# Performance work log

Hardware: AMD Instinct MI355X
Metric: run time of the kernel (lower is better)

The kernel has to match this reference:

```python
import jax, jax.numpy as jnp
import numpy as np

N, D, H, E = 4096, 512, 8, 131072
DH = D // H
BN_EPS = 1e-5


def setup_inputs() -> dict:
    key = jax.random.key(0)
    ks = jax.random.split(key, 12)
    def w(k, shape):
        return jax.random.normal(k, shape, dtype=jnp.float32) * 0.02
    return {
        'x': jax.random.normal(ks[0], (N, D), dtype=jnp.float32),
        'edge_index': jax.random.randint(ks[1], (2, E), 0, N),
        'edge_attr': jax.random.normal(ks[2], (E, D), dtype=jnp.float32),
        # GINE MLP: Linear(D,D) -> ReLU -> Linear(D,D)  (torch layout [out,in])
        'w_gin1': w(ks[3], (D, D)), 'b_gin1': jnp.zeros((D,), jnp.float32),
        'w_gin2': w(ks[4], (D, D)), 'b_gin2': jnp.zeros((D,), jnp.float32),
        # MultiheadAttention in/out projections
        'w_qkv': w(ks[5], (3 * D, D)), 'b_qkv': jnp.zeros((3 * D,), jnp.float32),
        'w_o': w(ks[6], (D, D)), 'b_o': jnp.zeros((D,), jnp.float32),
        # BatchNorm affine params
        'bn1l_g': jnp.ones((D,), jnp.float32), 'bn1l_b': jnp.zeros((D,), jnp.float32),
        'bn1a_g': jnp.ones((D,), jnp.float32), 'bn1a_b': jnp.zeros((D,), jnp.float32),
        # FFN: D -> 2D -> D
        'w_ff1': w(ks[7], (2 * D, D)), 'b_ff1': jnp.zeros((2 * D,), jnp.float32),
        'w_ff2': w(ks[8], (D, 2 * D)), 'b_ff2': jnp.zeros((D,), jnp.float32),
        'bn2_g': jnp.ones((D,), jnp.float32), 'bn2_b': jnp.zeros((D,), jnp.float32),
    }


def _bn(x, g, b):
    # BatchNorm1d in training mode: batch statistics over the node dim
    m = jnp.mean(x, axis=0)
    v = jnp.var(x, axis=0)
    return (x - m) * jax.lax.rsqrt(v + BN_EPS) * g + b


def _forward(x, edge_index, edge_attr,
             w_gin1, b_gin1, w_gin2, b_gin2,
             w_qkv, b_qkv, w_o, b_o,
             bn1l_g, bn1l_b, bn1a_g, bn1a_b,
             w_ff1, b_ff1, w_ff2, b_ff2, bn2_g, bn2_b):
    h_in = x
    src, dst = edge_index[0], edge_index[1]
    # --- local GINEConv: nn((1+eps)*x + sum_j relu(x_j + e_ji)), eps=0 ---
    msg = jax.nn.relu(x[src] + edge_attr)                       # [E, D]
    agg = jax.ops.segment_sum(msg, dst, num_segments=N)         # [N, D]
    gin_h = x + agg
    h_local = jax.nn.relu(gin_h @ w_gin1.T + b_gin1) @ w_gin2.T + b_gin2
    h_local = _bn(h_in + h_local, bn1l_g, bn1l_b)               # residual + BN
    # --- global multi-head self-attention over all nodes (single graph) ---
    qkv = x @ w_qkv.T + b_qkv                                   # [N, 3D]
    q, k, v = jnp.split(qkv, 3, axis=-1)
    q = q.reshape(N, H, DH).transpose(1, 0, 2)                  # [H, N, DH]
    k = k.reshape(N, H, DH).transpose(1, 0, 2)
    v = v.reshape(N, H, DH).transpose(1, 0, 2)
    scores = jnp.einsum('hnd,hmd->hnm', q, k) / np.float32(np.sqrt(DH))
    attn = jax.nn.softmax(scores, axis=-1)                      # [H, N, N]
    o = jnp.einsum('hnm,hmd->hnd', attn, v).transpose(1, 0, 2).reshape(N, D)
    h_attn = _bn(h_in + (o @ w_o.T + b_o), bn1a_g, bn1a_b)
    # --- combine branches + FFN block ---
    h = h_local + h_attn
    h = h + (jax.nn.relu(h @ w_ff1.T + b_ff1) @ w_ff2.T + b_ff2)
    return _bn(h, bn2_g, bn2_b)


def reference(x, edge_index, edge_attr,
              w_gin1, b_gin1, w_gin2, b_gin2,
              w_qkv, b_qkv, w_o, b_o,
              bn1l_g, bn1l_b, bn1a_g, bn1a_b,
              w_ff1, b_ff1, w_ff2, b_ff2, bn2_g, bn2_b):
    return _forward(x, edge_index, edge_attr,
                    w_gin1, b_gin1, w_gin2, b_gin2,
                    w_qkv, b_qkv, w_o, b_o,
                    bn1l_g, bn1l_b, bn1a_g, bn1a_b,
                    w_ff1, b_ff1, w_ff2, b_ff2, bn2_g, bn2_b)
```

## Files before the change

kernel.cpp:

```cpp
#include <hip/hip_runtime.h>

#define Nn 4096
#define Dd 512
#define Hh 8
#define Ee 131072
#define DEGCAP 96

typedef __attribute__((ext_vector_type(8))) short short8v;
typedef __attribute__((ext_vector_type(8))) unsigned short ushort8v;
typedef __attribute__((ext_vector_type(4))) short short4v;
typedef __attribute__((ext_vector_type(4))) float f32x4v;
typedef __attribute__((ext_vector_type(4))) unsigned short ushort4v;

__device__ __forceinline__ float bf2f(unsigned short u) {
    return __uint_as_float(((unsigned int)u) << 16);
}
__device__ __forceinline__ unsigned short f2bf(float f) {
    unsigned int u = __float_as_uint(f);
    return (unsigned short)((u + 0x7fff + ((u >> 16) & 1)) >> 16);
}
__device__ __forceinline__ void gl_lds16(const void* g, void* l) {
    __builtin_amdgcn_global_load_lds((const __attribute__((address_space(1))) void*)g,
                                     (__attribute__((address_space(3))) void*)l, 16, 0, 0);
}

struct CastJobs {
    const float* src[6];
    unsigned short* dst[6];
    int start[7];
    int* cnt;
    float* stats;
};

__global__ __launch_bounds__(256) void cast_multi(CastJobs cj) {
    int gid = blockIdx.x * 256 + threadIdx.x;
    if (gid < 4096) cj.cnt[gid] = 0;
    if (gid < 6144) cj.stats[gid] = 0.f;
    int b = blockIdx.x;
    int j = 0;
    while (b >= cj.start[j + 1]) j++;
    int off = (b - cj.start[j]) * 1024 + threadIdx.x * 4;
    f32x4v v = *(const f32x4v*)(cj.src[j] + off);
    ushort4v o;
    o.x = f2bf(v.x); o.y = f2bf(v.y); o.z = f2bf(v.z); o.w = f2bf(v.w);
    *(ushort4v*)(cj.dst[j] + off) = o;
}

__global__ __launch_bounds__(256) void edge_scatter(const int* __restrict__ ei,
                                                    int* __restrict__ cnt,
                                                    int* __restrict__ eidx) {
    int e = blockIdx.x * 256 + threadIdx.x;
    int d = ei[Ee + e];
    int pos = atomicAdd(&cnt[d], 1);
    if (pos < DEGCAP) eidx[d * DEGCAP + pos] = e;
}

__global__ __launch_bounds__(256) void gine_gather(const float* __restrict__ x,
                                                   const int* __restrict__ ei,
                                                   const float* __restrict__ ea,
                                                   const int* __restrict__ cnt,
                                                   const int* __restrict__ eidx,
                                                   unsigned short* __restrict__ gh,
                                                   unsigned short* __restrict__ xb) {
    __shared__ int se[DEGCAP];
    __shared__ int ss[DEGCAP];
    __shared__ float part[512];
    const int node = blockIdx.x;
    const int t = threadIdx.x;
    const int deg = min(cnt[node], DEGCAP);
    const int tc = t & 127, ep = t >> 7;

    if (t < deg) {
        int e = eidx[node * DEGCAP + t];
        se[t] = e;
        ss[t] = ei[e];
    }
    __syncthreads();

    f32x4v acc = {0.f, 0.f, 0.f, 0.f};
    int k = ep;
    while (k + 2 < deg) {
        int e0 = se[k], s0 = ss[k];
        int e1 = se[k + 2], s1 = ss[k + 2];
        f32x4v ev0 = *(const f32x4v*)(ea + (size_t)e0 * Dd + tc * 4);
        f32x4v xv0 = *(const f32x4v*)(x + (size_t)s0 * Dd + tc * 4);
        f32x4v ev1 = *(const f32x4v*)(ea + (size_t)e1 * Dd + tc * 4);
        f32x4v xv1 = *(const f32x4v*)(x + (size_t)s1 * Dd + tc * 4);
#pragma unroll
        for (int i = 0; i < 4; i++) {
            acc[i] += fmaxf(xv0[i] + ev0[i], 0.f);
            acc[i] += fmaxf(xv1[i] + ev1[i], 0.f);
        }
        k += 4;
    }
    if (k < deg) {
        int e0 = se[k], s0 = ss[k];
        f32x4v ev0 = *(const f32x4v*)(ea + (size_t)e0 * Dd + tc * 4);
        f32x4v xv0 = *(const f32x4v*)(x + (size_t)s0 * Dd + tc * 4);
#pragma unroll
        for (int i = 0; i < 4; i++) acc[i] += fmaxf(xv0[i] + ev0[i], 0.f);
    }

    if (ep) *(f32x4v*)&part[tc * 4] = acc;
    __syncthreads();
    if (!ep) {
        f32x4v o = *(const f32x4v*)&part[tc * 4];
        f32x4v xd = *(const f32x4v*)(x + (size_t)node * Dd + tc * 4);
        ushort4v ov, xv;
#pragma unroll
        for (int i = 0; i < 4; i++) {
            ov[i] = f2bf(xd[i] + acc[i] + o[i]);
            xv[i] = f2bf(xd[i]);
        }
        *(ushort4v*)(gh + (size_t)node * Dd + tc * 4) = ov;
        *(ushort4v*)(xb + (size_t)node * Dd + tc * 4) = xv;
    }
}

template <int K, int MB, bool RELU, bool OUTBF16, int RESMODE, bool SXADD, int SOFF, bool ACOMB>
__device__ __forceinline__ void gemm_body(char* smem,
                                          const short* __restrict__ A,
                                          const short* __restrict__ B,
                                          const float* __restrict__ bias,
                                          const void* __restrict__ res,
                                          void* __restrict__ outp, int Nc,
                                          const float* __restrict__ sx,
                                          float* __restrict__ stats,
                                          const unsigned short* __restrict__ op0,
                                          const unsigned short* __restrict__ op1,
                                          const unsigned short* __restrict__ op2,
                                          const unsigned short* __restrict__ op3,
                                          const float* __restrict__ lsum,
                                          int bx, int by, int t) {
    constexpr int BM = MB * 32;
    short* lA = (short*)smem;
    short* lB = (short*)(smem + MB * 2048);
    float* sst = (float*)(smem + MB * 2048 + 8192);
    const int lane = t & 63, w = t >> 6;
    const int wr = w >> 1, wc = w & 1;
    const int l15 = lane & 15, lhi = lane >> 4;
    const int m0 = by * BM, n0 = bx * 128;
    f32x4v acc[MB][4] = {};
    const int c0 = t, c1 = t + 256;

    for (int k0 = 0; k0 < K; k0 += 32) {
        __syncthreads();
        if constexpr (ACOMB) {
            int r = c0 >> 2, s = c0 & 3;
            int row = m0 + r;
            int kb = k0 + s * 8;
            int h = k0 >> 6;
            float inv = 1.f / (lsum[(size_t)h * Nn + row] + lsum[(size_t)(Hh + h) * Nn + row] +
                               lsum[(size_t)(2 * Hh + h) * Nn + row] + lsum[(size_t)(3 * Hh + h) * Nn + row]);
            ushort8v p0 = *(const ushort8v*)&op0[(size_t)row * 512 + kb];
            ushort8v p1 = *(const ushort8v*)&op1[(size_t)row * 512 + kb];
            ushort8v p2 = *(const ushort8v*)&op2[(size_t)row * 512 + kb];
            ushort8v p3 = *(const ushort8v*)&op3[(size_t)row * 512 + kb];
            short8v ov;
#pragma unroll
            for (int i = 0; i < 8; i++)
                ov[i] = (short)f2bf((bf2f(p0[i]) + bf2f(p1[i]) + bf2f(p2[i]) + bf2f(p3[i])) * inv);
            *(short8v*)((char*)lA + c0 * 16) = ov;
        } else {
            gl_lds16(A + (size_t)(m0 + (c0 >> 2)) * K + k0 + (c0 & 3) * 8, (char*)lA + c0 * 16);
            if constexpr (MB == 4)
                gl_lds16(A + (size_t)(m0 + (c1 >> 2)) * K + k0 + (c1 & 3) * 8, (char*)lA + c1 * 16);
        }
        gl_lds16(B + (size_t)(n0 + (c0 >> 2)) * K + k0 + (c0 & 3) * 8, (char*)lB + c0 * 16);
        gl_lds16(B + (size_t)(n0 + (c1 >> 2)) * K + k0 + (c1 & 3) * 8, (char*)lB + c1 * 16);
        __syncthreads();
        short8v af[MB], bf[4];
#pragma unroll
        for (int m = 0; m < MB; m++)
            af[m] = *(const short8v*)&lA[(wr * (MB * 16) + m * 16 + l15) * 32 + lhi * 8];
#pragma unroll
        for (int n = 0; n < 4; n++)
            bf[n] = *(const short8v*)&lB[(wc * 64 + n * 16 + l15) * 32 + lhi * 8];
#pragma unroll
        for (int m = 0; m < MB; m++)
#pragma unroll
            for (int n = 0; n < 4; n++)
                acc[m][n] = __builtin_amdgcn_mfma_f32_16x16x32_bf16(af[m], bf[n], acc[m][n], 0, 0, 0);
    }

    float csum[4] = {0.f, 0.f, 0.f, 0.f}, cssq[4] = {0.f, 0.f, 0.f, 0.f};

#pragma unroll
    for (int m = 0; m < MB; m++)
#pragma unroll
        for (int n = 0; n < 4; n++)
#pragma unroll
            for (int j = 0; j < 4; j++) {
                int col = n0 + wc * 64 + n * 16 + l15;
                int row = m0 + wr * (MB * 16) + m * 16 + lhi * 4 + j;
                size_t idx = (size_t)row * Nc + col;
                float v = acc[m][n][j] + bias[col];
                if (RELU) v = fmaxf(v, 0.f);
                if constexpr (RESMODE == 1) v += ((const float*)res)[idx];
                if constexpr (RESMODE == 2) v += bf2f(((const unsigned short*)res)[idx]);
                if constexpr (SOFF >= 0) {
                    float a = SXADD ? (sx[idx] + v) : v;
                    csum[n] += a;
                    cssq[n] += a * a;
                }
                if (OUTBF16)
                    ((unsigned short*)outp)[idx] = f2bf(v);
                else
                    ((float*)outp)[idx] = v;
            }

    if constexpr (SOFF >= 0) {
        sst[t] = 0.f;
        __syncthreads();
#pragma unroll
        for (int n = 0; n < 4; n++) {
            float s = csum[n], q = cssq[n];
            s += __shfl_xor(s, 16); s += __shfl_xor(s, 32);
            q += __shfl_xor(q, 16); q += __shfl_xor(q, 32);
            if (lhi == 0) {
                int c = wc * 64 + n * 16 + l15;
                atomicAdd(&sst[c * 2], s);
                atomicAdd(&sst[c * 2 + 1], q);
            }
        }
        __syncthreads();
        atomicAdd(&stats[SOFF + (t & 1) * 512 + n0 + (t >> 1)], sst[t]);
    }
}

__device__ __forceinline__ void attn_body(char* smem, const short* __restrict__ qkv,
                                          unsigned short* __restrict__ op0,
                                          unsigned short* __restrict__ op1,
                                          unsigned short* __restrict__ op2,
                                          unsigned short* __restrict__ op3,
                                          float* __restrict__ lsum,
                                          int bx, int by, int t) {
    const int lane = t & 63, w = t >> 6;
    const int h = by >> 2, quarter = by & 3;
    const int kvbase = quarter * 1024;
    const int qw = bx * 256 + w * 64;
    const int l15 = lane & 15, lhi = lane >> 4;
    const int ksw = l15 & 7;
    const int qs3 = (l15 >> 1) & 7;
    unsigned short* __restrict__ opart = quarter == 0 ? op0 : quarter == 1 ? op1 : quarter == 2 ? op2 : op3;

    short* pP = (short*)(smem + 32768) + w * 4096;

    short8v qf[4][2];
#pragma unroll
    for (int g = 0; g < 4; g++)
#pragma unroll
        for (int kk = 0; kk < 2; kk++)
            qf[g][kk] = *(const short8v*)&qkv[(size_t)(qw + g * 16 + l15) * 1536 + h * 64 + kk * 32 + lhi * 8];

    f32x4v oacc[4][4] = {};
    float lrow[4] = {0.f, 0.f, 0.f, 0.f};
    const float SC2 = 0.125f * 1.44269504f;

    int kidx[4][2];
#pragma unroll
    for (int r = 0; r < 4; r++)
#pragma unroll
        for (int kk = 0; kk < 2; kk++)
            kidx[r][kk] = (l15 + r * 16) * 64 + (((kk * 4 + lhi) ^ ksw) * 8);

    int pw_idx[4], prd_idx[2];
#pragma unroll
    for (int c2 = 0; c2 < 4; c2++)
        pw_idx[c2] = l15 * 64 + (((c2 * 2 + (lhi >> 1)) ^ qs3) * 8) + ((lhi & 1) * 4);
#pragma unroll
    for (int c = 0; c < 2; c++)
        prd_idx[c] = l15 * 64 + (((c * 4 + lhi) ^ qs3) * 8);

    unsigned vbase0 = (unsigned)(size_t)(smem + 16384) + lhi * 256 + l15 * 2;

    auto stage = [&](int kt, int b) {
        int kv0 = kvbase + kt * 64;
#pragma unroll
        for (int i = 0; i < 2; i++) {
            gl_lds16(qkv + (size_t)(kv0 + (t >> 3) + 32 * i) * 1536 + 512 + h * 64 + ((t & 7) ^ ((t >> 3) & 7)) * 8,
                     smem + b * 8192 + t * 16 + i * 4096);
        }
#pragma unroll
        for (int i = 0; i < 2; i++) {
            int db = (t >> 7) + 2 * i;
            int kv = (t >> 1) & 63;
            int dh_in = (t & 1) * 8;
            gl_lds16(qkv + (size_t)(kv0 + kv) * 1536 + 1024 + h * 64 + db * 16 + dh_in,
                     smem + 16384 + b * 8192 + t * 16 + i * 4096);
        }
    };

    stage(0, 0);
    __syncthreads();

    for (int kt = 0; kt < 16; kt++) {
        const int b = kt & 1;
        if (kt + 1 < 16) stage(kt + 1, b ^ 1);

        const short* Kb = (const short*)smem + b * 4096;
        const unsigned vbase = vbase0 + b * 8192;

        f32x4v s[4][4] = {};
        __builtin_amdgcn_s_setprio(1);
#pragma unroll
        for (int r = 0; r < 4; r++) {
            short8v k0 = *(const short8v*)&Kb[kidx[r][0]];
            short8v k1 = *(const short8v*)&Kb[kidx[r][1]];
#pragma unroll
            for (int g = 0; g < 4; g++) {
                s[g][r] = __builtin_amdgcn_mfma_f32_16x16x32_bf16(k0, qf[g][0], s[g][r], 0, 0, 0);
                s[g][r] = __builtin_amdgcn_mfma_f32_16x16x32_bf16(k1, qf[g][1], s[g][r], 0, 0, 0);
            }
        }
        __builtin_amdgcn_s_setprio(0);

#pragma unroll
        for (int g = 0; g < 4; g++) {
            float p[16];
            float rs = 0.f;
#pragma unroll
            for (int r = 0; r < 4; r++)
#pragma unroll
                for (int j = 0; j < 4; j++) {
                    float e = exp2f(fmaf(s[g][r][j], SC2, -4.f));
                    p[r * 4 + j] = e;
                    rs += e;
                }
            rs += __shfl_xor(rs, 16);
            rs += __shfl_xor(rs, 32);
            lrow[g] += rs;

            short* pPg = pP + g * 1024;
#pragma unroll
            for (int c2 = 0; c2 < 4; c2++) {
                short4v pk;
#pragma unroll
                for (int j = 0; j < 4; j++) pk[j] = (short)f2bf(p[c2 * 4 + j]);
                *(short4v*)&pPg[pw_idx[c2]] = pk;
            }
        }
        asm volatile("" ::: "memory");

        short8v pf[4][2];
#pragma unroll
        for (int g = 0; g < 4; g++)
#pragma unroll
            for (int c = 0; c < 2; c++)
                pf[g][c] = *(const short8v*)&pP[g * 1024 + prd_idx[c]];

        short4v v00a, v00b, v01a, v01b, v10a, v10b, v11a, v11b;
        short4v v20a, v20b, v21a, v21b, v30a, v30b, v31a, v31b;
        asm volatile("ds_read_b64_tr_b16 %0, %1" : "=v"(v00a) : "v"(vbase));
        asm volatile("ds_read_b64_tr_b16 %0, %1 offset:128" : "=v"(v00b) : "v"(vbase));
        asm volatile("ds_read_b64_tr_b16 %0, %1 offset:1024" : "=v"(v01a) : "v"(vbase));
        asm volatile("ds_read_b64_tr_b16 %0, %1 offset:1152" : "=v"(v01b) : "v"(vbase));
        asm volatile("ds_read_b64_tr_b16 %0, %1 offset:2048" : "=v"(v10a) : "v"(vbase));
        asm volatile("ds_read_b64_tr_b16 %0, %1 offset:2176" : "=v"(v10b) : "v"(vbase));
        asm volatile("ds_read_b64_tr_b16 %0, %1 offset:3072" : "=v"(v11a) : "v"(vbase));
        asm volatile("ds_read_b64_tr_b16 %0, %1 offset:3200" : "=v"(v11b) : "v"(vbase));
        asm volatile("ds_read_b64_tr_b16 %0, %1 offset:4096" : "=v"(v20a) : "v"(vbase));
        asm volatile("ds_read_b64_tr_b16 %0, %1 offset:4224" : "=v"(v20b) : "v"(vbase));
        asm volatile("ds_read_b64_tr_b16 %0, %1 offset:5120" : "=v"(v21a) : "v"(vbase));
        asm volatile("ds_read_b64_tr_b16 %0, %1 offset:5248" : "=v"(v21b) : "v"(vbase));
        asm volatile("ds_read_b64_tr_b16 %0, %1 offset:6144" : "=v"(v30a) : "v"(vbase));
        asm volatile("ds_read_b64_tr_b16 %0, %1 offset:6272" : "=v"(v30b) : "v"(vbase));
        asm volatile("ds_read_b64_tr_b16 %0, %1 offset:7168" : "=v"(v31a) : "v"(vbase));
        asm volatile("ds_read_b64_tr_b16 %0, %1 offset:7296" : "=v"(v31b) : "v"(vbase));

        asm volatile("s_waitcnt lgkmcnt(0)" ::: "memory");
        __builtin_amdgcn_sched_barrier(0);

#define VFCAT(a, b) __builtin_shufflevector(a, b, 0, 1, 2, 3, 4, 5, 6, 7)
        short8v vv[4][2];
        vv[0][0] = VFCAT(v00a, v00b); vv[0][1] = VFCAT(v01a, v01b);
        vv[1][0] = VFCAT(v10a, v10b); vv[1][1] = VFCAT(v11a, v11b);
        vv[2][0] = VFCAT(v20a, v20b); vv[2][1] = VFCAT(v21a, v21b);
        vv[3][0] = VFCAT(v30a, v30b); vv[3][1] = VFCAT(v31a, v31b);
#undef VFCAT
        __builtin_amdgcn_s_setprio(1);
#pragma unroll
        for (int g = 0; g < 4; g++)
#pragma unroll
            for (int n = 0; n < 4; n++) {
                oacc[g][n] = __builtin_amdgcn_mfma_f32_16x16x32_bf16(pf[g][0], vv[n][0], oacc[g][n], 0, 0, 0);
                oacc[g][n] = __builtin_amdgcn_mfma_f32_16x16x32_bf16(pf[g][1], vv[n][1], oacc[g][n], 0, 0, 0);
            }
        __builtin_amdgcn_s_setprio(0);

        __syncthreads();
    }

#pragma unroll
    for (int g = 0; g < 4; g++) {
#pragma unroll
        for (int j = 0; j < 4; j++) {
            int row = qw + g * 16 + lhi * 4 + j;
#pragma unroll
            for (int n = 0; n < 4; n++)
                opart[(size_t)row * Dd + h * 64 + n * 16 + l15] = f2bf(oacc[g][n][j]);
        }
        if (lhi == 0)
            lsum[(size_t)(quarter * Hh + h) * Nn + qw + g * 16 + l15] = lrow[g];
    }
}

__global__ __launch_bounds__(256) void gin1_qkv(const short* ginh, const short* wg1b,
                                                const float* b_gin1, unsigned short* t1,
                                                const short* xb, const short* wqkvb,
                                                const float* b_qkv, unsigned short* qkvb) {
    __shared__ char smem[16384];
    int b = blockIdx.x, t = threadIdx.x;
    if (b < 256) {
        gemm_body<512, 2, true, true, 0, false, -1, false>(
            smem, ginh, wg1b, b_gin1, nullptr, t1, 512, nullptr, nullptr,
            nullptr, nullptr, nullptr, nullptr, nullptr, b & 3, b >> 2, t);
    } else {
        int bb = b - 256;
        gemm_body<512, 4, false, true, 0, false, -1, false>(
            smem, xb, wqkvb, b_qkv, nullptr, qkvb, 1536, nullptr, nullptr,
            nullptr, nullptr, nullptr, nullptr, nullptr, bb % 12, bb / 12, t);
    }
}

__global__ __launch_bounds__(256, 2) void gin2_attn(const short* qkvb, unsigned short* op0,
                                                    unsigned short* op1, unsigned short* op2,
                                                    unsigned short* op3, float* lsum,
                                                    const short* t1, const short* wg2b,
                                                    const float* b_gin2, float* hlp,
                                                    const float* x, float* stats) {
    __shared__ char smem[65536];
    int b = blockIdx.x, t = threadIdx.x;
    if (b < 512) {
        attn_body(smem, qkvb, op0, op1, op2, op3, lsum, b & 15, b >> 4, t);
    } else {
        int bb = b - 512;
        gemm_body<512, 2, false, false, 0, true, 0, false>(
            smem, t1, wg2b, b_gin2, nullptr, hlp, 512, x, stats,
            nullptr, nullptr, nullptr, nullptr, nullptr, bb & 3, bb >> 2, t);
    }
}

__global__ __launch_bounds__(256) void oproj_fused(const short* wob, const float* b_o,
                                                   float* attn_pre, const float* x, float* stats,
                                                   const unsigned short* op0,
                                                   const unsigned short* op1,
                                                   const unsigned short* op2,
                                                   const unsigned short* op3,
                                                   const float* lsum) {
    __shared__ char smem[13312];
    gemm_body<512, 2, false, false, 0, true, 1024, true>(
        smem, nullptr, wob, b_o, nullptr, attn_pre, 512, x, stats,
        op0, op1, op2, op3, lsum, blockIdx.x, blockIdx.y, threadIdx.x);
}

__global__ __launch_bounds__(256) void ff1_k(const short* hb, const short* wf1b,
                                             const float* b_ff1, unsigned short* t2) {
    __shared__ char smem[16384];
    gemm_body<512, 4, true, true, 0, false, -1, false>(
        smem, hb, wf1b, b_ff1, nullptr, t2, 1024, nullptr, nullptr,
        nullptr, nullptr, nullptr, nullptr, nullptr, blockIdx.x, blockIdx.y, threadIdx.x);
}

__global__ __launch_bounds__(256) void ff2_k(const short* t2, const short* wf2b,
                                             const float* b_ff2, const unsigned short* hb,
                                             float* dout, float* stats) {
    __shared__ char smem[13312];
    gemm_body<1024, 2, false, false, 2, false, 4096, false>(
        smem, t2, wf2b, b_ff2, hb, dout, 512, nullptr, stats,
        nullptr, nullptr, nullptr, nullptr, nullptr, blockIdx.x, blockIdx.y, threadIdx.x);
}

__global__ __launch_bounds__(256) void bn_combine(const float* __restrict__ x,
                                                  const float* __restrict__ p1,
                                                  const float* __restrict__ p2,
                                                  const float* __restrict__ stats,
                                                  const float* __restrict__ g1,
                                                  const float* __restrict__ b1,
                                                  const float* __restrict__ g2,
                                                  const float* __restrict__ b2,
                                                  unsigned short* __restrict__ hb) {
    int i0 = (blockIdx.x * 256 + threadIdx.x) * 4;
    int c0 = i0 & 511;
    f32x4v xv = *(const f32x4v*)(x + i0);
    f32x4v av = *(const f32x4v*)(p1 + i0);
    f32x4v bv = *(const f32x4v*)(p2 + i0);
    ushort4v hbv;
#pragma unroll
    for (int e = 0; e < 4; e++) {
        int c = c0 + e;
        float ma = stats[c] * (1.f / Nn);
        float va = stats[512 + c] * (1.f / Nn) - ma * ma;
        float sA = g1[c] * rsqrtf(va + 1e-5f);
        float bA = b1[c] - ma * sA;
        float mb = stats[1024 + c] * (1.f / Nn);
        float vb = stats[1536 + c] * (1.f / Nn) - mb * mb;
        float sB = g2[c] * rsqrtf(vb + 1e-5f);
        float bB = b2[c] - mb * sB;
        float a = xv[e] + av[e];
        float b = xv[e] + bv[e];
        hbv[e] = f2bf(a * sA + bA + b * sB + bB);
    }
    *(ushort4v*)(hb + i0) = hbv;
}

__global__ __launch_bounds__(256) void bn_apply(float* __restrict__ out,
                                                const float* __restrict__ stats,
                                                const float* __restrict__ g,
                                                const float* __restrict__ b) {
    int i0 = (blockIdx.x * 256 + threadIdx.x) * 4;
    int c0 = i0 & 511;
    f32x4v v = *(const f32x4v*)(out + i0);
#pragma unroll
    for (int e = 0; e < 4; e++) {
        int c = c0 + e;
        float m = stats[4096 + c] * (1.f / Nn);
        float va = stats[4608 + c] * (1.f / Nn) - m * m;
        float s = g[c] * rsqrtf(va + 1e-5f);
        v[e] = (v[e] - m) * s + b[c];
    }
    *(f32x4v*)(out + i0) = v;
}

extern "C" void kernel_launch(void* const* d_in, const int* in_sizes, int n_in,
                              void* d_out, int out_size, void* d_ws, size_t ws_size,
                              hipStream_t stream) {
    const float* x = (const float*)d_in[0];
    const int* ei = (const int*)d_in[1];
    const float* ea = (const float*)d_in[2];
    const float* w_gin1 = (const float*)d_in[3];
    const float* b_gin1 = (const float*)d_in[4];
    const float* w_gin2 = (const float*)d_in[5];
    const float* b_gin2 = (const float*)d_in[6];
    const float* w_qkv = (const float*)d_in[7];
    const float* b_qkv = (const float*)d_in[8];
    const float* w_o = (const float*)d_in[9];
    const float* b_o = (const float*)d_in[10];
    const float* bn1l_g = (const float*)d_in[11];
    const float* bn1l_b = (const float*)d_in[12];
    const float* bn1a_g = (const float*)d_in[13];
    const float* bn1a_b = (const float*)d_in[14];
    const float* w_ff1 = (const float*)d_in[15];
    const float* b_ff1 = (const float*)d_in[16];
    const float* w_ff2 = (const float*)d_in[17];
    const float* b_ff2 = (const float*)d_in[18];
    const float* bn2_g = (const float*)d_in[19];
    const float* bn2_b = (const float*)d_in[20];

    char* ws = (char*)d_ws;
    unsigned short* wg1b = (unsigned short*)(ws + 0);
    unsigned short* wg2b = (unsigned short*)(ws + 524288);
    unsigned short* wqkvb = (unsigned short*)(ws + 1048576);
    unsigned short* wob = (unsigned short*)(ws + 2621440);
    unsigned short* wf1b = (unsigned short*)(ws + 3145728);
    unsigned short* wf2b = (unsigned short*)(ws + 4194304);
    unsigned short* xb = (unsigned short*)(ws + 5242880);
    unsigned short* qkvb = (unsigned short*)(ws + 9437184);
    int* eidx = (int*)(ws + 22020096);
    int* cnt = (int*)(ws + 23592960);
    unsigned short* ginh = (unsigned short*)(ws + 30408704);
    float* lsum = (float*)(ws + 30408704);
    unsigned short* t1 = (unsigned short*)(ws + 34603008);
    float* hlp = (float*)(ws + 38797312);
    unsigned short* opart2 = (unsigned short*)(ws + 47185920);
    float* attn_pre = (float*)(ws + 51380224);
    unsigned short* opart0 = (unsigned short*)(ws + 59768832);
    unsigned short* hb = (unsigned short*)(ws + 68157440);
    unsigned short* opart3 = (unsigned short*)(ws + 68157440);
    unsigned short* t2 = (unsigned short*)(ws + 72351744);
    unsigned short* opart1 = (unsigned short*)(ws + 72351744);
    float* stats = (float*)(ws + 80740352);

    CastJobs cj;
    cj.src[0] = w_gin1; cj.dst[0] = wg1b;
    cj.src[1] = w_gin2; cj.dst[1] = wg2b;
    cj.src[2] = w_qkv;  cj.dst[2] = wqkvb;
    cj.src[3] = w_o;    cj.dst[3] = wob;
    cj.src[4] = w_ff1;  cj.dst[4] = wf1b;
    cj.src[5] = w_ff2;  cj.dst[5] = wf2b;
    cj.cnt = cnt;
    cj.stats = stats;
    int nelem[6] = {Dd * Dd, Dd * Dd, 3 * Dd * Dd, Dd * Dd, 2 * Dd * Dd, 2 * Dd * Dd};
    cj.start[0] = 0;
    for (int i = 0; i < 6; i++) cj.start[i + 1] = cj.start[i] + nelem[i] / 1024;
    cast_multi<<<cj.start[6], 256, 0, stream>>>(cj);

    edge_scatter<<<Ee / 256, 256, 0, stream>>>(ei, cnt, eidx);
    gine_gather<<<Nn, 256, 0, stream>>>(x, ei, ea, cnt, eidx, ginh, xb);

    gin1_qkv<<<640, 256, 0, stream>>>((const short*)ginh, (const short*)wg1b, b_gin1, t1,
                                      (const short*)xb, (const short*)wqkvb, b_qkv, qkvb);

    gin2_attn<<<768, 256, 0, stream>>>((const short*)qkvb, opart0, opart1, opart2, opart3, lsum,
                                       (const short*)t1, (const short*)wg2b, b_gin2, hlp,
                                       x, stats);

    oproj_fused<<<dim3(4, 64), 256, 0, stream>>>((const short*)wob, b_o, attn_pre, x, stats,
                                                 opart0, opart1, opart2, opart3, lsum);

    bn_combine<<<Nn * Dd / 1024, 256, 0, stream>>>(x, hlp, attn_pre, stats,
                                                   bn1l_g, bn1l_b, bn1a_g, bn1a_b, hb);

    ff1_k<<<dim3(8, 32), 256, 0, stream>>>((const short*)hb, (const short*)wf1b, b_ff1, t2);
    ff2_k<<<dim3(4, 64), 256, 0, stream>>>((const short*)t2, (const short*)wf2b, b_ff2,
                                           hb, (float*)d_out, stats);

    bn_apply<<<Nn * Dd / 1024, 256, 0, stream>>>((float*)d_out, stats, bn2_g, bn2_b);
}
```

Before: 257.2 us.

## Load attention K fragments directly from global into registers, shrink LDS

Each wave now loads its K-tile MFMA operands straight from global memory into double-buffered registers, prefetching the next tile, instead of staging K through LDS. Only V is still staged in LDS, so shared memory drops from 64KB to 48KB and the P buffer moves down. Launch bounds lose the minimum-2-blocks hint. This removes the LDS writes and reads for K, but each wave now issues redundant global/L2 reads of K and uses more registers, which may lower occupancy.

```diff
diff --git a/kernel.cpp b/kernel.cpp
--- a/kernel.cpp
+++ b/kernel.cpp
@@ -240,11 +240,10 @@
     const int kvbase = quarter * 1024;
     const int qw = bx * 256 + w * 64;
     const int l15 = lane & 15, lhi = lane >> 4;
-    const int ksw = l15 & 7;
     const int qs3 = (l15 >> 1) & 7;
     unsigned short* __restrict__ opart = quarter == 0 ? op0 : quarter == 1 ? op1 : quarter == 2 ? op2 : op3;
 
-    short* pP = (short*)(smem + 32768) + w * 4096;
+    short* pP = (short*)(smem + 16384) + w * 4096;
 
     short8v qf[4][2];
 #pragma unroll
@@ -257,12 +256,12 @@
     float lrow[4] = {0.f, 0.f, 0.f, 0.f};
     const float SC2 = 0.125f * 1.44269504f;
 
-    int kidx[4][2];
+    const short* kp[4][2];
 #pragma unroll
     for (int r = 0; r < 4; r++)
 #pragma unroll
         for (int kk = 0; kk < 2; kk++)
-            kidx[r][kk] = (l15 + r * 16) * 64 + (((kk * 4 + lhi) ^ ksw) * 8);
+            kp[r][kk] = qkv + (size_t)(kvbase + l15 + r * 16) * 1536 + 512 + h * 64 + kk * 32 + lhi * 8;
 
     int pw_idx[4], prd_idx[2];
 #pragma unroll
@@ -272,47 +271,49 @@
     for (int c = 0; c < 2; c++)
         prd_idx[c] = l15 * 64 + (((c * 4 + lhi) ^ qs3) * 8);
 
-    unsigned vbase0 = (unsigned)(size_t)(smem + 16384) + lhi * 256 + l15 * 2;
-
-    auto stage = [&](int kt, int b) {
+    unsigned vbase0 = (unsigned)(size_t)smem + lhi * 256 + l15 * 2;
+
+    auto stageV = [&](int kt, int b) {
         int kv0 = kvbase + kt * 64;
-#pragma unroll
-        for (int i = 0; i < 2; i++) {
-            gl_lds16(qkv + (size_t)(kv0 + (t >> 3) + 32 * i) * 1536 + 512 + h * 64 + ((t & 7) ^ ((t >> 3) & 7)) * 8,
-                     smem + b * 8192 + t * 16 + i * 4096);
-        }
 #pragma unroll
         for (int i = 0; i < 2; i++) {
             int db = (t >> 7) + 2 * i;
             int kv = (t >> 1) & 63;
             int dh_in = (t & 1) * 8;
             gl_lds16(qkv + (size_t)(kv0 + kv) * 1536 + 1024 + h * 64 + db * 16 + dh_in,
-                     smem + 16384 + b * 8192 + t * 16 + i * 4096);
+                     smem + b * 8192 + t * 16 + i * 4096);
         }
     };
-
-    stage(0, 0);
+    auto loadK = [&](int kt, short8v (&kf)[4][2]) {
+        size_t roff = (size_t)kt * 64 * 1536;
+#pragma unroll
+        for (int r = 0; r < 4; r++)
+#pragma unroll
+            for (int kk = 0; kk < 2; kk++)
+                kf[r][kk] = *(const short8v*)(kp[r][kk] + roff);
+    };
+
+    short8v kfA[4][2], kfB[4][2];
+    loadK(0, kfA);
+    stageV(0, 0);
     __syncthreads();
 
-    for (int kt = 0; kt < 16; kt++) {
-        const int b = kt & 1;
-        if (kt + 1 < 16) stage(kt + 1, b ^ 1);
-
-        const short* Kb = (const short*)smem + b * 4096;
+    auto body = [&](int kt, int b, short8v (&kfC)[4][2], short8v (&kfN)[4][2]) {
+        if (kt + 1 < 16) {
+            loadK(kt + 1, kfN);
+            stageV(kt + 1, b ^ 1);
+        }
         const unsigned vbase = vbase0 + b * 8192;
 
         f32x4v s[4][4] = {};
         __builtin_amdgcn_s_setprio(1);
 #pragma unroll
-        for (int r = 0; r < 4; r++) {
-            short8v k0 = *(const short8v*)&Kb[kidx[r][0]];
-            short8v k1 = *(const short8v*)&Kb[kidx[r][1]];
+        for (int r = 0; r < 4; r++)
 #pragma unroll
             for (int g = 0; g < 4; g++) {
-                s[g][r] = __builtin_amdgcn_mfma_f32_16x16x32_bf16(k0, qf[g][0], s[g][r], 0, 0, 0);
-                s[g][r] = __builtin_amdgcn_mfma_f32_16x16x32_bf16(k1, qf[g][1], s[g][r], 0, 0, 0);
+                s[g][r] = __builtin_amdgcn_mfma_f32_16x16x32_bf16(kfC[r][0], qf[g][0], s[g][r], 0, 0, 0);
+                s[g][r] = __builtin_amdgcn_mfma_f32_16x16x32_bf16(kfC[r][1], qf[g][1], s[g][r], 0, 0, 0);
             }
-        }
         __builtin_amdgcn_s_setprio(0);
 
 #pragma unroll
@@ -389,6 +390,11 @@
         __builtin_amdgcn_s_setprio(0);
 
         __syncthreads();
+    };
+
+    for (int kt2 = 0; kt2 < 8; kt2++) {
+        body(2 * kt2, 0, kfA, kfB);
+        body(2 * kt2 + 1, 1, kfB, kfA);
     }
 
 #pragma unroll
@@ -423,13 +429,13 @@
     }
 }
 
-__global__ __launch_bounds__(256, 2) void gin2_attn(const short* qkvb, unsigned short* op0,
-                                                    unsigned short* op1, unsigned short* op2,
-                                                    unsigned short* op3, float* lsum,
-                                                    const short* t1, const short* wg2b,
-                                                    const float* b_gin2, float* hlp,
-                                                    const float* x, float* stats) {
-    __shared__ char smem[65536];
+__global__ __launch_bounds__(256) void gin2_attn(const short* qkvb, unsigned short* op0,
+                                                 unsigned short* op1, unsigned short* op2,
+                                                 unsigned short* op3, float* lsum,
+                                                 const short* t1, const short* wg2b,
+                                                 const float* b_gin2, float* hlp,
+                                                 const float* x, float* stats) {
+    __shared__ char smem[49152];
     int b = blockIdx.x, t = threadIdx.x;
     if (b < 512) {
         attn_body(smem, qkvb, op0, op1, op2, op3, lsum, b & 15, b >> 4, t);
```

Result: slower. 297.4 us (+15.7%).
